# Performance work log

Hardware: AMD Instinct MI355X
Metric: run time of the kernel (lower is better)

Reference implementation:

```python
import jax, jax.numpy as jnp
import numpy as np

N_NODES = 20000
N_EDGES = 320000
IN_F = 256
OUT_F = 256
EDGE_F = 256


def _mlp2(x, W1, b1, W2, b2):
    # MLPLayers(2, [d_in, 2*d_in, d_out]) = Linear -> ReLU -> Linear
    return jax.nn.relu(x @ W1 + b1) @ W2 + b2


def setup_inputs() -> dict:
    key = jax.random.key(0)
    ks = jax.random.split(key, 12)

    def lin(k, fan_in, shape):
        bound = 1.0 / np.sqrt(fan_in)
        return jax.random.uniform(k, shape, jnp.float32, -bound, bound)

    node_feat = jax.random.normal(ks[0], (N_NODES, IN_F), jnp.float32)
    edge_feat = jax.random.normal(ks[1], (N_EDGES, EDGE_F), jnp.float32)
    src = jax.random.randint(ks[2], (N_EDGES,), 0, N_NODES, jnp.int32)
    dst = jax.random.randint(ks[3], (N_EDGES,), 0, N_NODES, jnp.int32)

    # edge_mlp: edge_feats -> 2*edge_feats -> in_feats
    We1 = lin(ks[4], EDGE_F, (EDGE_F, 2 * EDGE_F))
    be1 = lin(ks[5], EDGE_F, (2 * EDGE_F,))
    We2 = lin(ks[6], 2 * EDGE_F, (2 * EDGE_F, IN_F))
    be2 = lin(ks[7], 2 * EDGE_F, (IN_F,))
    # node mlp: in_feats -> 2*in_feats -> out_feats
    Wn1 = lin(ks[8], IN_F, (IN_F, 2 * IN_F))
    bn1 = lin(ks[9], IN_F, (2 * IN_F,))
    Wn2 = lin(ks[10], 2 * IN_F, (2 * IN_F, OUT_F))
    bn2 = lin(ks[11], 2 * IN_F, (OUT_F,))
    eps = jnp.zeros((1,), jnp.float32)

    return {"node_feat": node_feat, "edge_feat": edge_feat, "src": src, "dst": dst,
            "We1": We1, "be1": be1, "We2": We2, "be2": be2,
            "Wn1": Wn1, "bn1": bn1, "Wn2": Wn2, "bn2": bn2, "eps": eps}


def reference(node_feat, edge_feat, src, dst, We1, be1, We2, be2, Wn1, bn1, Wn2, bn2, eps):
    e = _mlp2(edge_feat, We1, be1, We2, be2)            # [E, IN_F]
    msg = jax.nn.relu(node_feat[src] + e)               # gather-add-relu
    out_h = jax.ops.segment_sum(msg, dst, num_segments=N_NODES)  # [N, IN_F]
    out = _mlp2((1.0 + eps[0]) * node_feat + out_h, Wn1, bn1, Wn2, bn2)
    return out
```

## Files before the change

kernel.cpp:

```cpp
#include <hip/hip_runtime.h>

#define NN  20000
#define NE  320000
#define FIN 256
#define FH  512

typedef __attribute__((ext_vector_type(8))) short bf16x8;
typedef __attribute__((ext_vector_type(4))) float f32x4;
typedef __attribute__((ext_vector_type(4))) unsigned short u16x4;

static __device__ __forceinline__ unsigned short f2b(float f) {
    union { float f; unsigned int i; } v; v.f = f;
    return (unsigned short)((v.i + 0x7fffu + ((v.i >> 16) & 1u)) >> 16);
}
static __device__ __forceinline__ f32x4 mfma16(bf16x8 a, bf16x8 b, f32x4 c) {
    return __builtin_amdgcn_mfma_f32_16x16x32_bf16(a, b, c, 0, 0, 0);
}
static __device__ __forceinline__ u16x4 pack4(float a, float b, float c, float d) {
    u16x4 p;
    p[0] = f2b(a); p[1] = f2b(b); p[2] = f2b(c); p[3] = f2b(d);
    return p;
}

__global__ void prep_weights(const float* __restrict__ We1, const float* __restrict__ We2,
                             const float* __restrict__ Wn1, const float* __restrict__ Wn2,
                             unsigned short* __restrict__ W1T, unsigned short* __restrict__ W2T,
                             unsigned short* __restrict__ Wn1T, unsigned short* __restrict__ Wn2T) {
    const int m = blockIdx.x >> 7;
    const int t = blockIdx.x & 127;
    const float* src; unsigned short* dst; int R, C;
    if      (m == 0) { src = We1; dst = W1T;  R = 256; C = 512; }
    else if (m == 1) { src = We2; dst = W2T;  R = 512; C = 256; }
    else if (m == 2) { src = Wn1; dst = Wn1T; R = 256; C = 512; }
    else             { src = Wn2; dst = Wn2T; R = 512; C = 256; }
    __shared__ unsigned short tl[32][33];
    const int tx  = threadIdx.x & 31;
    const int tyb = threadIdx.x >> 5;
    const int cb = C >> 5;
    const int bx = t % cb, by = t / cb;
    #pragma unroll
    for (int j = 0; j < 4; ++j)
        tl[tyb * 4 + j][tx] = f2b(src[(size_t)(by * 32 + tyb * 4 + j) * C + bx * 32 + tx]);
    __syncthreads();
    #pragma unroll
    for (int j = 0; j < 4; ++j)
        dst[(size_t)(bx * 32 + tyb * 4 + j) * R + by * 32 + tx] = tl[tx][tyb * 4 + j];
}

__global__ void hist_dst(const int* __restrict__ dstI, int* __restrict__ cnt) {
    int e = blockIdx.x * 256 + threadIdx.x;
    if (e < NE) atomicAdd(&cnt[dstI[e]], 1);
}

__global__ void scan_excl(const int* __restrict__ cnt, int* __restrict__ cursor) {
    __shared__ int c[NN];
    __shared__ int s[1024];
    const int t = threadIdx.x;
    for (int i = t; i < NN; i += 1024) c[i] = cnt[i];
    __syncthreads();
    const int lo = t * 20;
    const int hi = (lo + 20 < NN) ? lo + 20 : NN;
    int sum = 0;
    for (int i = lo; i < hi; ++i) sum += c[i];
    s[t] = sum;
    __syncthreads();
    for (int off = 1; off < 1024; off <<= 1) {
        int v = (t >= off) ? s[t - off] : 0;
        __syncthreads();
        s[t] += v;
        __syncthreads();
    }
    int base = (t > 0) ? s[t - 1] : 0;
    for (int i = lo; i < hi; ++i) { int cv = c[i]; c[i] = base; base += cv; }
    __syncthreads();
    for (int i = t; i < NN; i += 1024) cursor[i] = c[i];
}

__global__ void scatter_perm(const int* __restrict__ dstI,
                             int* __restrict__ cursor, int* __restrict__ perm) {
    int e = blockIdx.x * 256 + threadIdx.x;
    if (e < NE) {
        int pos = atomicAdd(&cursor[dstI[e]], 1);
        perm[pos] = e;
    }
}

__global__ void __launch_bounds__(512, 4)
gine_edge(const float* __restrict__ edge_feat,
          const float* __restrict__ node_feat,
          const int* __restrict__ srcI,
          const int* __restrict__ dstI,
          const int* __restrict__ perm,
          const unsigned short* __restrict__ W1T,
          const float* __restrict__ b1,
          const unsigned short* __restrict__ W2T,
          const float* __restrict__ b2,
          float* __restrict__ out_h)
{
    __shared__ union {
        unsigned short Xs[64 * 264];
        unsigned short Hs[64 * 512];
        float          Msg[64 * 260];
    } sh;
    __shared__ int snS[64], dnS[64], eS[64];

    const int tid  = threadIdx.x;
    const int wave = tid >> 6;
    const int lane = tid & 63;
    const int quad = lane >> 4;
    const int ln   = lane & 15;
    const int bs   = (blockIdx.x & 7) * 625 + (blockIdx.x >> 3);
    const int e0   = bs * 64;

    if (tid < 64) {
        const int e = perm[e0 + tid];
        eS[tid]  = e;
        snS[tid] = srcI[e];
        dnS[tid] = dstI[e];
    }
    __syncthreads();

    #pragma unroll
    for (int it = 0; it < 4; ++it) {
        const int chunk = tid + it * 512;
        const int row = chunk >> 5;
        const int c8  = (chunk & 31) << 3;
        const float* p = edge_feat + (size_t)eS[row] * FIN + c8;
        f32x4 o0 = *(const f32x4*)(p);
        f32x4 o1 = *(const f32x4*)(p + 4);
        bf16x8 pack;
        #pragma unroll
        for (int j = 0; j < 4; ++j) {
            pack[j]     = (short)f2b(o0[j]);
            pack[j + 4] = (short)f2b(o1[j]);
        }
        *(bf16x8*)(&sh.Xs[row * 264 + c8]) = pack;
    }
    __syncthreads();

    f32x4 zero4 = {0.f, 0.f, 0.f, 0.f};
    f32x4 acc1[4][4];
    #pragma unroll
    for (int nt = 0; nt < 4; ++nt)
        #pragma unroll
        for (int et = 0; et < 4; ++et) acc1[nt][et] = zero4;

    const unsigned short* wB = W1T + (wave * 64 + ln) * FIN + quad * 8;
    #pragma unroll
    for (int ks = 0; ks < 8; ++ks) {
        bf16x8 w[4], x[4];
        #pragma unroll
        for (int nt = 0; nt < 4; ++nt)
            w[nt] = *(const bf16x8*)(wB + nt * 16 * FIN + ks * 32);
        #pragma unroll
        for (int et = 0; et < 4; ++et)
            x[et] = *(const bf16x8*)(&sh.Xs[(et * 16 + ln) * 264 + quad * 8 + ks * 32]);
        #pragma unroll
        for (int nt = 0; nt < 4; ++nt)
            #pragma unroll
            for (int et = 0; et < 4; ++et)
                acc1[nt][et] = mfma16(w[nt], x[et], acc1[nt][et]);
    }
    __syncthreads();

    #pragma unroll
    for (int nt = 0; nt < 4; ++nt) {
        const int n0 = wave * 64 + nt * 16 + quad * 4;
        const f32x4 b4 = *(const f32x4*)(b1 + n0);
        #pragma unroll
        for (int et = 0; et < 4; ++et) {
            const int edge = et * 16 + ln;
            u16x4 p = pack4(fmaxf(acc1[nt][et][0] + b4[0], 0.f),
                            fmaxf(acc1[nt][et][1] + b4[1], 0.f),
                            fmaxf(acc1[nt][et][2] + b4[2], 0.f),
                            fmaxf(acc1[nt][et][3] + b4[3], 0.f));
            *(u16x4*)(&sh.Hs[(edge << 9) + (((n0 >> 3) ^ (edge & 7)) << 3) + (n0 & 7)]) = p;
        }
    }
    __syncthreads();

    f32x4 acc2[2][4];
    #pragma unroll
    for (int nt = 0; nt < 2; ++nt)
        #pragma unroll
        for (int et = 0; et < 4; ++et) acc2[nt][et] = zero4;

    const unsigned short* w2B = W2T + (wave * 32 + ln) * FH;
    #pragma unroll
    for (int ks = 0; ks < 16; ++ks) {
        const int kb = ks * 4 + quad;
        bf16x8 w[2], h[4];
        #pragma unroll
        for (int nt = 0; nt < 2; ++nt)
            w[nt] = *(const bf16x8*)(w2B + nt * 16 * FH + kb * 8);
        #pragma unroll
        for (int et = 0; et < 4; ++et) {
            const int edge = et * 16 + ln;
            h[et] = *(const bf16x8*)(&sh.Hs[(edge << 9) + ((kb ^ (edge & 7)) << 3)]);
        }
        #pragma unroll
        for (int nt = 0; nt < 2; ++nt)
            #pragma unroll
            for (int et = 0; et < 4; ++et)
                acc2[nt][et] = mfma16(w[nt], h[et], acc2[nt][et]);
    }
    __syncthreads();

    #pragma unroll
    for (int nt = 0; nt < 2; ++nt) {
        const int n0 = wave * 32 + nt * 16 + quad * 4;
        const f32x4 b4 = *(const f32x4*)(b2 + n0);
        #pragma unroll
        for (int et = 0; et < 4; ++et) {
            const int edge = et * 16 + ln;
            const int sn = snS[edge];
            const f32x4 nf = *(const f32x4*)(node_feat + (size_t)sn * FIN + n0);
            f32x4 m;
            #pragma unroll
            for (int r = 0; r < 4; ++r)
                m[r] = fmaxf(nf[r] + acc2[nt][et][r] + b4[r], 0.f);
            *(f32x4*)(&sh.Msg[edge * 260 + n0]) = m;
        }
    }
    __syncthreads();

    {
        const int col  = tid & 255;
        const int half = tid >> 8;
        const int rA   = half * 32;
        const int dF = dnS[rA], dL = dnS[rA + 31];
        float run = sh.Msg[rA * 260 + col];
        int cur = dF;
        #pragma unroll 4
        for (int row = rA + 1; row < rA + 32; ++row) {
            const int d = dnS[row];
            if (d != cur) {
                if (cur == dF || cur == dL)
                    atomicAdd(&out_h[(size_t)cur * FIN + col], run);
                else
                    out_h[(size_t)cur * FIN + col] = run;
                run = 0.f;
                cur = d;
            }
            run += sh.Msg[row * 260 + col];
        }
        atomicAdd(&out_h[(size_t)cur * FIN + col], run);
    }
}

__global__ void __launch_bounds__(512, 4)
gine_node(const float* __restrict__ node_feat,
          const float* __restrict__ out_h,
          const unsigned short* __restrict__ W1T,
          const float* __restrict__ b1,
          const unsigned short* __restrict__ W2T,
          const float* __restrict__ b2,
          const float* __restrict__ eps,
          float* __restrict__ out)
{
    __shared__ union {
        unsigned short Xs[64 * 264];
        unsigned short Hs[64 * 512];
    } sh;

    const int tid  = threadIdx.x;
    const int wave = tid >> 6;
    const int lane = tid & 63;
    const int quad = lane >> 4;
    const int ln   = lane & 15;
    const int n0b  = blockIdx.x * 64;
    const float epsv = 1.0f + eps[0];

    #pragma unroll
    for (int it = 0; it < 4; ++it) {
        const int chunk = tid + it * 512;
        const int row = chunk >> 5;
        const int c8  = (chunk & 31) << 3;
        const int g   = n0b + row;
        bf16x8 pack = {0, 0, 0, 0, 0, 0, 0, 0};
        if (g < NN) {
            const float* pn = node_feat + (size_t)g * FIN + c8;
            const float* ph = out_h + (size_t)g * FIN + c8;
            f32x4 n0v = *(const f32x4*)(pn);
            f32x4 n1v = *(const f32x4*)(pn + 4);
            f32x4 h0v = *(const f32x4*)(ph);
            f32x4 h1v = *(const f32x4*)(ph + 4);
            #pragma unroll
            for (int j = 0; j < 4; ++j) {
                pack[j]     = (short)f2b(epsv * n0v[j] + h0v[j]);
                pack[j + 4] = (short)f2b(epsv * n1v[j] + h1v[j]);
            }
        }
        *(bf16x8*)(&sh.Xs[row * 264 + c8]) = pack;
    }
    __syncthreads();

    f32x4 zero4 = {0.f, 0.f, 0.f, 0.f};
    f32x4 acc1[4][4];
    #pragma unroll
    for (int nt = 0; nt < 4; ++nt)
        #pragma unroll
        for (int et = 0; et < 4; ++et) acc1[nt][et] = zero4;

    const unsigned short* wB = W1T + (wave * 64 + ln) * FIN + quad * 8;
    #pragma unroll
    for (int ks = 0; ks < 8; ++ks) {
        bf16x8 w[4], x[4];
        #pragma unroll
        for (int nt = 0; nt < 4; ++nt)
            w[nt] = *(const bf16x8*)(wB + nt * 16 * FIN + ks * 32);
        #pragma unroll
        for (int et = 0; et < 4; ++et)
            x[et] = *(const bf16x8*)(&sh.Xs[(et * 16 + ln) * 264 + quad * 8 + ks * 32]);
        #pragma unroll
        for (int nt = 0; nt < 4; ++nt)
            #pragma unroll
            for (int et = 0; et < 4; ++et)
                acc1[nt][et] = mfma16(w[nt], x[et], acc1[nt][et]);
    }
    __syncthreads();

    #pragma unroll
    for (int nt = 0; nt < 4; ++nt) {
        const int n0 = wave * 64 + nt * 16 + quad * 4;
        const f32x4 b4 = *(const f32x4*)(b1 + n0);
        #pragma unroll
        for (int et = 0; et < 4; ++et) {
            const int edge = et * 16 + ln;
            u16x4 p = pack4(fmaxf(acc1[nt][et][0] + b4[0], 0.f),
                            fmaxf(acc1[nt][et][1] + b4[1], 0.f),
                            fmaxf(acc1[nt][et][2] + b4[2], 0.f),
                            fmaxf(acc1[nt][et][3] + b4[3], 0.f));
            *(u16x4*)(&sh.Hs[(edge << 9) + (((n0 >> 3) ^ (edge & 7)) << 3) + (n0 & 7)]) = p;
        }
    }
    __syncthreads();

    f32x4 acc2[2][4];
    #pragma unroll
    for (int nt = 0; nt < 2; ++nt)
        #pragma unroll
        for (int et = 0; et < 4; ++et) acc2[nt][et] = zero4;

    const unsigned short* w2B = W2T + (wave * 32 + ln) * FH;
    #pragma unroll
    for (int ks = 0; ks < 16; ++ks) {
        const int kb = ks * 4 + quad;
        bf16x8 w[2], h[4];
        #pragma unroll
        for (int nt = 0; nt < 2; ++nt)
            w[nt] = *(const bf16x8*)(w2B + nt * 16 * FH + kb * 8);
        #pragma unroll
        for (int et = 0; et < 4; ++et) {
            const int edge = et * 16 + ln;
            h[et] = *(const bf16x8*)(&sh.Hs[(edge << 9) + ((kb ^ (edge & 7)) << 3)]);
        }
        #pragma unroll
        for (int nt = 0; nt < 2; ++nt)
            #pragma unroll
            for (int et = 0; et < 4; ++et)
                acc2[nt][et] = mfma16(w[nt], h[et], acc2[nt][et]);
    }

    #pragma unroll
    for (int nt = 0; nt < 2; ++nt) {
        const int n0 = wave * 32 + nt * 16 + quad * 4;
        const f32x4 b4 = *(const f32x4*)(b2 + n0);
        #pragma unroll
        for (int et = 0; et < 4; ++et) {
            const int g = n0b + et * 16 + ln;
            if (g < NN) {
                f32x4 o;
                #pragma unroll
                for (int r = 0; r < 4; ++r)
                    o[r] = acc2[nt][et][r] + b4[r];
                *(f32x4*)(out + (size_t)g * FIN + n0) = o;
            }
        }
    }
}

extern "C" void kernel_launch(void* const* d_in, const int* in_sizes, int n_in,
                              void* d_out, int out_size, void* d_ws, size_t ws_size,
                              hipStream_t stream) {
    const float* node_feat = (const float*)d_in[0];
    const float* edge_feat = (const float*)d_in[1];
    const int* srcI = (const int*)d_in[2];
    const int* dstI = (const int*)d_in[3];
    const float* We1 = (const float*)d_in[4];
    const float* be1 = (const float*)d_in[5];
    const float* We2 = (const float*)d_in[6];
    const float* be2 = (const float*)d_in[7];
    const float* Wn1 = (const float*)d_in[8];
    const float* bn1 = (const float*)d_in[9];
    const float* Wn2 = (const float*)d_in[10];
    const float* bn2 = (const float*)d_in[11];
    const float* eps = (const float*)d_in[12];

    char* ws = (char*)d_ws;
    float* out_h = (float*)ws;
    unsigned short* W1T  = (unsigned short*)(ws + 20480000);
    unsigned short* W2T  = W1T + 131072;
    unsigned short* Wn1T = W2T + 131072;
    unsigned short* Wn2T = Wn1T + 131072;
    int* cnt    = (int*)(ws + 20480000 + 4 * 262144);
    int* cursor = cnt + NN;
    int* perm   = cursor + NN;

    hipMemsetAsync(out_h, 0, (size_t)NN * FIN * sizeof(float), stream);
    hipMemsetAsync(cnt, 0, NN * sizeof(int), stream);

    prep_weights<<<512, 256, 0, stream>>>(We1, We2, Wn1, Wn2, W1T, W2T, Wn1T, Wn2T);

    hist_dst<<<(NE + 255) / 256, 256, 0, stream>>>(dstI, cnt);
    scan_excl<<<1, 1024, 0, stream>>>(cnt, cursor);
    scatter_perm<<<(NE + 255) / 256, 256, 0, stream>>>(dstI, cursor, perm);

    gine_edge<<<NE / 64, 512, 0, stream>>>(edge_feat, node_feat, srcI, dstI,
                                           perm, W1T, be1, W2T, be2, out_h);
    gine_node<<<(NN + 63) / 64, 512, 0, stream>>>(node_feat, out_h, Wn1T, bn1,
                                                  Wn2T, bn2, eps, (float*)d_out);
}
```

Baseline: 870.5 us.

## Make edge kernel persistent with prefetched indices and direct fp32 edge-feature loads

The edge kernel becomes persistent: 512 blocks each loop over 9-10 tiles of 64 edges, and the next tile's perm/src/dst indices are prefetched into a double-buffered shared array. The shared Xs staging of edge features is removed. Each lane now loads its fp32 edge-feature slice straight from global memory and converts it in registers with packed bf16 conversion before the MFMA, which drops a shared round trip and a barrier. In exchange there are fewer resident blocks, so less latency hiding, and the gathered global loads become less coalesced (32-byte pieces per lane).

```diff
diff --git a/kernel.cpp b/kernel.cpp
--- a/kernel.cpp
+++ b/kernel.cpp
@@ -1,4 +1,5 @@
 #include <hip/hip_runtime.h>
+#include <hip/hip_bf16.h>
 
 #define NN  20000
 #define NE  320000
@@ -8,6 +9,7 @@
 typedef __attribute__((ext_vector_type(8))) short bf16x8;
 typedef __attribute__((ext_vector_type(4))) float f32x4;
 typedef __attribute__((ext_vector_type(4))) unsigned short u16x4;
+typedef __attribute__((ext_vector_type(4))) unsigned int u32x4;
 
 static __device__ __forceinline__ unsigned short f2b(float f) {
     union { float f; unsigned int i; } v; v.f = f;
@@ -20,6 +22,19 @@
     u16x4 p;
     p[0] = f2b(a); p[1] = f2b(b); p[2] = f2b(c); p[3] = f2b(d);
     return p;
+}
+static __device__ __forceinline__ unsigned int cvtpk(float lo, float hi) {
+    union { __hip_bfloat162 h; unsigned int u; } v;
+    v.h = __float22bfloat162_rn(float2{lo, hi});
+    return v.u;
+}
+static __device__ __forceinline__ bf16x8 cvt8(f32x4 a, f32x4 b) {
+    u32x4 t;
+    t[0] = cvtpk(a[0], a[1]);
+    t[1] = cvtpk(a[2], a[3]);
+    t[2] = cvtpk(b[0], b[1]);
+    t[3] = cvtpk(b[2], b[3]);
+    return __builtin_bit_cast(bf16x8, t);
 }
 
 __global__ void prep_weights(const float* __restrict__ We1, const float* __restrict__ We2,
@@ -98,153 +113,160 @@
           float* __restrict__ out_h)
 {
     __shared__ union {
-        unsigned short Xs[64 * 264];
         unsigned short Hs[64 * 512];
         float          Msg[64 * 260];
     } sh;
-    __shared__ int snS[64], dnS[64], eS[64];
+    __shared__ int snS[2][64], dnS[2][64], eS[2][64];
 
     const int tid  = threadIdx.x;
     const int wave = tid >> 6;
     const int lane = tid & 63;
     const int quad = lane >> 4;
     const int ln   = lane & 15;
-    const int bs   = (blockIdx.x & 7) * 625 + (blockIdx.x >> 3);
-    const int e0   = bs * 64;
+
+    const int x = blockIdx.x & 7;
+    const int j = blockIdx.x >> 3;
+    const int off   = (j < 49) ? j * 10 : 490 + (j - 49) * 9;
+    const int ntile = (j < 49) ? 10 : 9;
+    const int t0    = x * 625 + off;
 
     if (tid < 64) {
-        const int e = perm[e0 + tid];
-        eS[tid]  = e;
-        snS[tid] = srcI[e];
-        dnS[tid] = dstI[e];
-    }
-    __syncthreads();
-
-    #pragma unroll
-    for (int it = 0; it < 4; ++it) {
-        const int chunk = tid + it * 512;
-        const int row = chunk >> 5;
-        const int c8  = (chunk & 31) << 3;
-        const float* p = edge_feat + (size_t)eS[row] * FIN + c8;
-        f32x4 o0 = *(const f32x4*)(p);
-        f32x4 o1 = *(const f32x4*)(p + 4);
-        bf16x8 pack;
-        #pragma unroll
-        for (int j = 0; j < 4; ++j) {
-            pack[j]     = (short)f2b(o0[j]);
-            pack[j + 4] = (short)f2b(o1[j]);
-        }
-        *(bf16x8*)(&sh.Xs[row * 264 + c8]) = pack;
-    }
-    __syncthreads();
-
-    f32x4 zero4 = {0.f, 0.f, 0.f, 0.f};
-    f32x4 acc1[4][4];
-    #pragma unroll
-    for (int nt = 0; nt < 4; ++nt)
-        #pragma unroll
-        for (int et = 0; et < 4; ++et) acc1[nt][et] = zero4;
-
-    const unsigned short* wB = W1T + (wave * 64 + ln) * FIN + quad * 8;
-    #pragma unroll
-    for (int ks = 0; ks < 8; ++ks) {
-        bf16x8 w[4], x[4];
+        const int e = perm[t0 * 64 + tid];
+        eS[0][tid] = e; snS[0][tid] = srcI[e]; dnS[0][tid] = dstI[e];
+    }
+    __syncthreads();
+
+    const unsigned short* wB  = W1T + (wave * 64 + ln) * FIN + quad * 8;
+    const unsigned short* w2B = W2T + (wave * 32 + ln) * FH;
+    const f32x4 zero4 = {0.f, 0.f, 0.f, 0.f};
+
+    for (int i = 0; i < ntile; ++i) {
+        const int p  = i & 1;
+        const int q  = p ^ 1;
+
+        int eN = 0, sN = 0, dN = 0;
+        const bool pf = (tid < 64) && (i + 1 < ntile);
+        if (pf) {
+            eN = perm[(t0 + i + 1) * 64 + tid];
+            sN = srcI[eN];
+            dN = dstI[eN];
+        }
+
+        const float* xb[4];
+        #pragma unroll
+        for (int et = 0; et < 4; ++et)
+            xb[et] = edge_feat + (size_t)eS[p][et * 16 + ln] * FIN + quad * 8;
+
+        f32x4 acc1[4][4];
         #pragma unroll
         for (int nt = 0; nt < 4; ++nt)
-            w[nt] = *(const bf16x8*)(wB + nt * 16 * FIN + ks * 32);
-        #pragma unroll
-        for (int et = 0; et < 4; ++et)
-            x[et] = *(const bf16x8*)(&sh.Xs[(et * 16 + ln) * 264 + quad * 8 + ks * 32]);
-        #pragma unroll
-        for (int nt = 0; nt < 4; ++nt)
-            #pragma unroll
-            for (int et = 0; et < 4; ++et)
-                acc1[nt][et] = mfma16(w[nt], x[et], acc1[nt][et]);
-    }
-    __syncthreads();
-
-    #pragma unroll
-    for (int nt = 0; nt < 4; ++nt) {
-        const int n0 = wave * 64 + nt * 16 + quad * 4;
-        const f32x4 b4 = *(const f32x4*)(b1 + n0);
-        #pragma unroll
-        for (int et = 0; et < 4; ++et) {
-            const int edge = et * 16 + ln;
-            u16x4 p = pack4(fmaxf(acc1[nt][et][0] + b4[0], 0.f),
-                            fmaxf(acc1[nt][et][1] + b4[1], 0.f),
-                            fmaxf(acc1[nt][et][2] + b4[2], 0.f),
-                            fmaxf(acc1[nt][et][3] + b4[3], 0.f));
-            *(u16x4*)(&sh.Hs[(edge << 9) + (((n0 >> 3) ^ (edge & 7)) << 3) + (n0 & 7)]) = p;
-        }
-    }
-    __syncthreads();
-
-    f32x4 acc2[2][4];
-    #pragma unroll
-    for (int nt = 0; nt < 2; ++nt)
-        #pragma unroll
-        for (int et = 0; et < 4; ++et) acc2[nt][et] = zero4;
-
-    const unsigned short* w2B = W2T + (wave * 32 + ln) * FH;
-    #pragma unroll
-    for (int ks = 0; ks < 16; ++ks) {
-        const int kb = ks * 4 + quad;
-        bf16x8 w[2], h[4];
+            #pragma unroll
+            for (int et = 0; et < 4; ++et) acc1[nt][et] = zero4;
+
+        #pragma unroll
+        for (int ks = 0; ks < 8; ++ks) {
+            bf16x8 w[4], xf[4];
+            #pragma unroll
+            for (int nt = 0; nt < 4; ++nt)
+                w[nt] = *(const bf16x8*)(wB + nt * 16 * FIN + ks * 32);
+            #pragma unroll
+            for (int et = 0; et < 4; ++et) {
+                const f32x4 a = *(const f32x4*)(xb[et] + ks * 32);
+                const f32x4 b = *(const f32x4*)(xb[et] + ks * 32 + 4);
+                xf[et] = cvt8(a, b);
+            }
+            #pragma unroll
+            for (int nt = 0; nt < 4; ++nt)
+                #pragma unroll
+                for (int et = 0; et < 4; ++et)
+                    acc1[nt][et] = mfma16(w[nt], xf[et], acc1[nt][et]);
+        }
+
+        if (pf) { eS[q][tid] = eN; snS[q][tid] = sN; dnS[q][tid] = dN; }
+
+        #pragma unroll
+        for (int nt = 0; nt < 4; ++nt) {
+            const int n0 = wave * 64 + nt * 16 + quad * 4;
+            const f32x4 b4 = *(const f32x4*)(b1 + n0);
+            #pragma unroll
+            for (int et = 0; et < 4; ++et) {
+                const int edge = et * 16 + ln;
+                u16x4 pk = pack4(fmaxf(acc1[nt][et][0] + b4[0], 0.f),
+                                 fmaxf(acc1[nt][et][1] + b4[1], 0.f),
+                                 fmaxf(acc1[nt][et][2] + b4[2], 0.f),
+                                 fmaxf(acc1[nt][et][3] + b4[3], 0.f));
+                *(u16x4*)(&sh.Hs[(edge << 9) + (((n0 >> 3) ^ (edge & 7)) << 3) + (n0 & 7)]) = pk;
+            }
+        }
+        __syncthreads();
+
+        f32x4 acc2[2][4];
         #pragma unroll
         for (int nt = 0; nt < 2; ++nt)
-            w[nt] = *(const bf16x8*)(w2B + nt * 16 * FH + kb * 8);
-        #pragma unroll
-        for (int et = 0; et < 4; ++et) {
-            const int edge = et * 16 + ln;
-            h[et] = *(const bf16x8*)(&sh.Hs[(edge << 9) + ((kb ^ (edge & 7)) << 3)]);
-        }
-        #pragma unroll
-        for (int nt = 0; nt < 2; ++nt)
-            #pragma unroll
-            for (int et = 0; et < 4; ++et)
-                acc2[nt][et] = mfma16(w[nt], h[et], acc2[nt][et]);
-    }
-    __syncthreads();
-
-    #pragma unroll
-    for (int nt = 0; nt < 2; ++nt) {
-        const int n0 = wave * 32 + nt * 16 + quad * 4;
-        const f32x4 b4 = *(const f32x4*)(b2 + n0);
-        #pragma unroll
-        for (int et = 0; et < 4; ++et) {
-            const int edge = et * 16 + ln;
-            const int sn = snS[edge];
-            const f32x4 nf = *(const f32x4*)(node_feat + (size_t)sn * FIN + n0);
-            f32x4 m;
-            #pragma unroll
-            for (int r = 0; r < 4; ++r)
-                m[r] = fmaxf(nf[r] + acc2[nt][et][r] + b4[r], 0.f);
-            *(f32x4*)(&sh.Msg[edge * 260 + n0]) = m;
-        }
-    }
-    __syncthreads();
-
-    {
-        const int col  = tid & 255;
-        const int half = tid >> 8;
-        const int rA   = half * 32;
-        const int dF = dnS[rA], dL = dnS[rA + 31];
-        float run = sh.Msg[rA * 260 + col];
-        int cur = dF;
-        #pragma unroll 4
-        for (int row = rA + 1; row < rA + 32; ++row) {
-            const int d = dnS[row];
-            if (d != cur) {
-                if (cur == dF || cur == dL)
-                    atomicAdd(&out_h[(size_t)cur * FIN + col], run);
-                else
-                    out_h[(size_t)cur * FIN + col] = run;
-                run = 0.f;
-                cur = d;
-            }
-            run += sh.Msg[row * 260 + col];
-        }
-        atomicAdd(&out_h[(size_t)cur * FIN + col], run);
+            #pragma unroll
+            for (int et = 0; et < 4; ++et) acc2[nt][et] = zero4;
+
+        #pragma unroll
+        for (int ks = 0; ks < 16; ++ks) {
+            const int kb = ks * 4 + quad;
+            bf16x8 w[2], h[4];
+            #pragma unroll
+            for (int nt = 0; nt < 2; ++nt)
+                w[nt] = *(const bf16x8*)(w2B + nt * 16 * FH + kb * 8);
+            #pragma unroll
+            for (int et = 0; et < 4; ++et) {
+                const int edge = et * 16 + ln;
+                h[et] = *(const bf16x8*)(&sh.Hs[(edge << 9) + ((kb ^ (edge & 7)) << 3)]);
+            }
+            #pragma unroll
+            for (int nt = 0; nt < 2; ++nt)
+                #pragma unroll
+                for (int et = 0; et < 4; ++et)
+                    acc2[nt][et] = mfma16(w[nt], h[et], acc2[nt][et]);
+        }
+        __syncthreads();
+
+        #pragma unroll
+        for (int nt = 0; nt < 2; ++nt) {
+            const int n0 = wave * 32 + nt * 16 + quad * 4;
+            const f32x4 b4 = *(const f32x4*)(b2 + n0);
+            #pragma unroll
+            for (int et = 0; et < 4; ++et) {
+                const int edge = et * 16 + ln;
+                const int sn = snS[p][edge];
+                const f32x4 nf = *(const f32x4*)(node_feat + (size_t)sn * FIN + n0);
+                f32x4 m;
+                #pragma unroll
+                for (int r = 0; r < 4; ++r)
+                    m[r] = fmaxf(nf[r] + acc2[nt][et][r] + b4[r], 0.f);
+                *(f32x4*)(&sh.Msg[edge * 260 + n0]) = m;
+            }
+        }
+        __syncthreads();
+
+        {
+            const int col  = tid & 255;
+            const int half = tid >> 8;
+            const int rA   = half * 32;
+            const int dF = dnS[p][rA], dL = dnS[p][rA + 31];
+            float run = sh.Msg[rA * 260 + col];
+            int cur = dF;
+            #pragma unroll 4
+            for (int row = rA + 1; row < rA + 32; ++row) {
+                const int d = dnS[p][row];
+                if (d != cur) {
+                    if (cur == dF || cur == dL)
+                        atomicAdd(&out_h[(size_t)cur * FIN + col], run);
+                    else
+                        out_h[(size_t)cur * FIN + col] = run;
+                    run = 0.f;
+                    cur = d;
+                }
+                run += sh.Msg[row * 260 + col];
+            }
+            atomicAdd(&out_h[(size_t)cur * FIN + col], run);
+        }
+        __syncthreads();
     }
 }
 
@@ -305,18 +327,18 @@
     const unsigned short* wB = W1T + (wave * 64 + ln) * FIN + quad * 8;
     #pragma unroll
     for (int ks = 0; ks < 8; ++ks) {
-        bf16x8 w[4], x[4];
+        bf16x8 w[4], xv[4];
         #pragma unroll
         for (int nt = 0; nt < 4; ++nt)
             w[nt] = *(const bf16x8*)(wB + nt * 16 * FIN + ks * 32);
         #pragma unroll
         for (int et = 0; et < 4; ++et)
-            x[et] = *(const bf16x8*)(&sh.Xs[(et * 16 + ln) * 264 + quad * 8 + ks * 32]);
+            xv[et] = *(const bf16x8*)(&sh.Xs[(et * 16 + ln) * 264 + quad * 8 + ks * 32]);
         #pragma unroll
         for (int nt = 0; nt < 4; ++nt)
             #pragma unroll
             for (int et = 0; et < 4; ++et)
-                acc1[nt][et] = mfma16(w[nt], x[et], acc1[nt][et]);
+                acc1[nt][et] = mfma16(w[nt], xv[et], acc1[nt][et]);
     }
     __syncthreads();
 
@@ -327,11 +349,11 @@
         #pragma unroll
         for (int et = 0; et < 4; ++et) {
             const int edge = et * 16 + ln;
-            u16x4 p = pack4(fmaxf(acc1[nt][et][0] + b4[0], 0.f),
-                            fmaxf(acc1[nt][et][1] + b4[1], 0.f),
-                            fmaxf(acc1[nt][et][2] + b4[2], 0.f),
-                            fmaxf(acc1[nt][et][3] + b4[3], 0.f));
-            *(u16x4*)(&sh.Hs[(edge << 9) + (((n0 >> 3) ^ (edge & 7)) << 3) + (n0 & 7)]) = p;
+            u16x4 pk = pack4(fmaxf(acc1[nt][et][0] + b4[0], 0.f),
+                             fmaxf(acc1[nt][et][1] + b4[1], 0.f),
+                             fmaxf(acc1[nt][et][2] + b4[2], 0.f),
+                             fmaxf(acc1[nt][et][3] + b4[3], 0.f));
+            *(u16x4*)(&sh.Hs[(edge << 9) + (((n0 >> 3) ^ (edge & 7)) << 3) + (n0 & 7)]) = pk;
         }
     }
     __syncthreads();
@@ -416,8 +438,8 @@
     scan_excl<<<1, 1024, 0, stream>>>(cnt, cursor);
     scatter_perm<<<(NE + 255) / 256, 256, 0, stream>>>(dstI, cursor, perm);
 
-    gine_edge<<<NE / 64, 512, 0, stream>>>(edge_feat, node_feat, srcI, dstI,
-                                           perm, W1T, be1, W2T, be2, out_h);
+    gine_edge<<<512, 512, 0, stream>>>(edge_feat, node_feat, srcI, dstI,
+                                       perm, W1T, be1, W2T, be2, out_h);
     gine_node<<<(NN + 63) / 64, 512, 0, stream>>>(node_feat, out_h, Wn1T, bn1,
                                                   Wn2T, bn2, eps, (float*)d_out);
 }
```

Measured after the change: 1.469 ms. 68.7% more time.

## Split hidden dimension into halves to shrink LDS and raise occupancy

Applied to the files above, without the earlier changes.

Both the edge and node MLP kernels now process the 512-wide hidden layer in two 256-wide halves, accumulating the second GEMM across halves. This halves the hidden-activation shared buffer and the first-layer accumulator registers. The message buffer is also processed in two 32-edge passes, so launch bounds can request 8 blocks per CU instead of 4. The input tile is cached in registers (xr[8][4]) and reused across halves, and the float-to-bf16 conversion now uses the packed hardware conversion intrinsic. The risks are extra barriers, re-reading W1 per half, and register pressure from holding the input tile.

```diff
diff --git a/kernel.cpp b/kernel.cpp
--- a/kernel.cpp
+++ b/kernel.cpp
@@ -1,4 +1,5 @@
 #include <hip/hip_runtime.h>
+#include <hip/hip_bf16.h>
 
 #define NN  20000
 #define NE  320000
@@ -8,6 +9,7 @@
 typedef __attribute__((ext_vector_type(8))) short bf16x8;
 typedef __attribute__((ext_vector_type(4))) float f32x4;
 typedef __attribute__((ext_vector_type(4))) unsigned short u16x4;
+typedef __attribute__((ext_vector_type(4))) unsigned int u32x4;
 
 static __device__ __forceinline__ unsigned short f2b(float f) {
     union { float f; unsigned int i; } v; v.f = f;
@@ -16,10 +18,23 @@
 static __device__ __forceinline__ f32x4 mfma16(bf16x8 a, bf16x8 b, f32x4 c) {
     return __builtin_amdgcn_mfma_f32_16x16x32_bf16(a, b, c, 0, 0, 0);
 }
+static __device__ __forceinline__ unsigned int cvtpk(float lo, float hi) {
+    union { __hip_bfloat162 h; unsigned int u; } v;
+    v.h = __float22bfloat162_rn(float2{lo, hi});
+    return v.u;
+}
 static __device__ __forceinline__ u16x4 pack4(float a, float b, float c, float d) {
-    u16x4 p;
-    p[0] = f2b(a); p[1] = f2b(b); p[2] = f2b(c); p[3] = f2b(d);
-    return p;
+    union { u16x4 s; unsigned int u[2]; } v;
+    v.u[0] = cvtpk(a, b); v.u[1] = cvtpk(c, d);
+    return v.s;
+}
+static __device__ __forceinline__ bf16x8 cvt8(f32x4 a, f32x4 b) {
+    u32x4 t;
+    t[0] = cvtpk(a[0], a[1]);
+    t[1] = cvtpk(a[2], a[3]);
+    t[2] = cvtpk(b[0], b[1]);
+    t[3] = cvtpk(b[2], b[3]);
+    return __builtin_bit_cast(bf16x8, t);
 }
 
 __global__ void prep_weights(const float* __restrict__ We1, const float* __restrict__ We2,
@@ -85,7 +100,7 @@
     }
 }
 
-__global__ void __launch_bounds__(512, 4)
+__global__ void __launch_bounds__(512, 8)
 gine_edge(const float* __restrict__ edge_feat,
           const float* __restrict__ node_feat,
           const int* __restrict__ srcI,
@@ -99,8 +114,8 @@
 {
     __shared__ union {
         unsigned short Xs[64 * 264];
-        unsigned short Hs[64 * 512];
-        float          Msg[64 * 260];
+        unsigned short Hs[64 * 256];
+        float          Msg[32 * 264];
     } sh;
     __shared__ int snS[64], dnS[64], eS[64];
 
@@ -128,127 +143,132 @@
         const float* p = edge_feat + (size_t)eS[row] * FIN + c8;
         f32x4 o0 = *(const f32x4*)(p);
         f32x4 o1 = *(const f32x4*)(p + 4);
-        bf16x8 pack;
-        #pragma unroll
-        for (int j = 0; j < 4; ++j) {
-            pack[j]     = (short)f2b(o0[j]);
-            pack[j + 4] = (short)f2b(o1[j]);
-        }
-        *(bf16x8*)(&sh.Xs[row * 264 + c8]) = pack;
-    }
-    __syncthreads();
-
-    f32x4 zero4 = {0.f, 0.f, 0.f, 0.f};
-    f32x4 acc1[4][4];
-    #pragma unroll
-    for (int nt = 0; nt < 4; ++nt)
-        #pragma unroll
-        for (int et = 0; et < 4; ++et) acc1[nt][et] = zero4;
-
-    const unsigned short* wB = W1T + (wave * 64 + ln) * FIN + quad * 8;
-    #pragma unroll
-    for (int ks = 0; ks < 8; ++ks) {
-        bf16x8 w[4], x[4];
-        #pragma unroll
-        for (int nt = 0; nt < 4; ++nt)
-            w[nt] = *(const bf16x8*)(wB + nt * 16 * FIN + ks * 32);
+        *(bf16x8*)(&sh.Xs[row * 264 + c8]) = cvt8(o0, o1);
+    }
+    __syncthreads();
+
+    bf16x8 xr[8][4];
+    #pragma unroll
+    for (int ks = 0; ks < 8; ++ks)
         #pragma unroll
         for (int et = 0; et < 4; ++et)
-            x[et] = *(const bf16x8*)(&sh.Xs[(et * 16 + ln) * 264 + quad * 8 + ks * 32]);
-        #pragma unroll
-        for (int nt = 0; nt < 4; ++nt)
-            #pragma unroll
-            for (int et = 0; et < 4; ++et)
-                acc1[nt][et] = mfma16(w[nt], x[et], acc1[nt][et]);
-    }
-    __syncthreads();
-
-    #pragma unroll
-    for (int nt = 0; nt < 4; ++nt) {
-        const int n0 = wave * 64 + nt * 16 + quad * 4;
-        const f32x4 b4 = *(const f32x4*)(b1 + n0);
-        #pragma unroll
-        for (int et = 0; et < 4; ++et) {
-            const int edge = et * 16 + ln;
-            u16x4 p = pack4(fmaxf(acc1[nt][et][0] + b4[0], 0.f),
-                            fmaxf(acc1[nt][et][1] + b4[1], 0.f),
-                            fmaxf(acc1[nt][et][2] + b4[2], 0.f),
-                            fmaxf(acc1[nt][et][3] + b4[3], 0.f));
-            *(u16x4*)(&sh.Hs[(edge << 9) + (((n0 >> 3) ^ (edge & 7)) << 3) + (n0 & 7)]) = p;
-        }
-    }
-    __syncthreads();
-
+            xr[ks][et] = *(const bf16x8*)(&sh.Xs[(et * 16 + ln) * 264 + quad * 8 + ks * 32]);
+    __syncthreads();
+
+    const f32x4 zero4 = {0.f, 0.f, 0.f, 0.f};
     f32x4 acc2[2][4];
     #pragma unroll
     for (int nt = 0; nt < 2; ++nt)
         #pragma unroll
         for (int et = 0; et < 4; ++et) acc2[nt][et] = zero4;
 
-    const unsigned short* w2B = W2T + (wave * 32 + ln) * FH;
-    #pragma unroll
-    for (int ks = 0; ks < 16; ++ks) {
-        const int kb = ks * 4 + quad;
-        bf16x8 w[2], h[4];
+    #pragma unroll
+    for (int h = 0; h < 2; ++h) {
+        f32x4 acc1[2][4];
         #pragma unroll
         for (int nt = 0; nt < 2; ++nt)
-            w[nt] = *(const bf16x8*)(w2B + nt * 16 * FH + kb * 8);
-        #pragma unroll
-        for (int et = 0; et < 4; ++et) {
-            const int edge = et * 16 + ln;
-            h[et] = *(const bf16x8*)(&sh.Hs[(edge << 9) + ((kb ^ (edge & 7)) << 3)]);
-        }
-        #pragma unroll
-        for (int nt = 0; nt < 2; ++nt)
-            #pragma unroll
-            for (int et = 0; et < 4; ++et)
-                acc2[nt][et] = mfma16(w[nt], h[et], acc2[nt][et]);
-    }
-    __syncthreads();
-
-    #pragma unroll
-    for (int nt = 0; nt < 2; ++nt) {
-        const int n0 = wave * 32 + nt * 16 + quad * 4;
-        const f32x4 b4 = *(const f32x4*)(b2 + n0);
-        #pragma unroll
-        for (int et = 0; et < 4; ++et) {
-            const int edge = et * 16 + ln;
-            const int sn = snS[edge];
-            const f32x4 nf = *(const f32x4*)(node_feat + (size_t)sn * FIN + n0);
-            f32x4 m;
-            #pragma unroll
-            for (int r = 0; r < 4; ++r)
-                m[r] = fmaxf(nf[r] + acc2[nt][et][r] + b4[r], 0.f);
-            *(f32x4*)(&sh.Msg[edge * 260 + n0]) = m;
-        }
-    }
-    __syncthreads();
-
-    {
-        const int col  = tid & 255;
-        const int half = tid >> 8;
-        const int rA   = half * 32;
-        const int dF = dnS[rA], dL = dnS[rA + 31];
-        float run = sh.Msg[rA * 260 + col];
-        int cur = dF;
-        #pragma unroll 4
-        for (int row = rA + 1; row < rA + 32; ++row) {
-            const int d = dnS[row];
-            if (d != cur) {
-                if (cur == dF || cur == dL)
-                    atomicAdd(&out_h[(size_t)cur * FIN + col], run);
-                else
-                    out_h[(size_t)cur * FIN + col] = run;
-                run = 0.f;
-                cur = d;
-            }
-            run += sh.Msg[row * 260 + col];
-        }
-        atomicAdd(&out_h[(size_t)cur * FIN + col], run);
-    }
-}
-
-__global__ void __launch_bounds__(512, 4)
+            #pragma unroll
+            for (int et = 0; et < 4; ++et) acc1[nt][et] = zero4;
+
+        const unsigned short* wB = W1T + (size_t)(h * 256 + wave * 32 + ln) * FIN + quad * 8;
+        #pragma unroll
+        for (int ks = 0; ks < 8; ++ks) {
+            bf16x8 w1[2];
+            #pragma unroll
+            for (int nt = 0; nt < 2; ++nt)
+                w1[nt] = *(const bf16x8*)(wB + nt * 16 * FIN + ks * 32);
+            #pragma unroll
+            for (int nt = 0; nt < 2; ++nt)
+                #pragma unroll
+                for (int et = 0; et < 4; ++et)
+                    acc1[nt][et] = mfma16(w1[nt], xr[ks][et], acc1[nt][et]);
+        }
+
+        #pragma unroll
+        for (int nt = 0; nt < 2; ++nt) {
+            const int nl = wave * 32 + nt * 16 + quad * 4;
+            const f32x4 b4 = *(const f32x4*)(b1 + h * 256 + nl);
+            #pragma unroll
+            for (int et = 0; et < 4; ++et) {
+                const int edge = et * 16 + ln;
+                u16x4 pk = pack4(fmaxf(acc1[nt][et][0] + b4[0], 0.f),
+                                 fmaxf(acc1[nt][et][1] + b4[1], 0.f),
+                                 fmaxf(acc1[nt][et][2] + b4[2], 0.f),
+                                 fmaxf(acc1[nt][et][3] + b4[3], 0.f));
+                *(u16x4*)(&sh.Hs[(edge << 8) + (((nl >> 3) ^ (edge & 7)) << 3) + (nl & 7)]) = pk;
+            }
+        }
+        __syncthreads();
+
+        const unsigned short* w2B = W2T + (size_t)(wave * 32 + ln) * FH + h * 256;
+        #pragma unroll
+        for (int ks = 0; ks < 8; ++ks) {
+            const int kb = ks * 4 + quad;
+            bf16x8 w2[2], hf[4];
+            #pragma unroll
+            for (int nt = 0; nt < 2; ++nt)
+                w2[nt] = *(const bf16x8*)(w2B + nt * 16 * FH + kb * 8);
+            #pragma unroll
+            for (int et = 0; et < 4; ++et) {
+                const int edge = et * 16 + ln;
+                hf[et] = *(const bf16x8*)(&sh.Hs[(edge << 8) + ((kb ^ (edge & 7)) << 3)]);
+            }
+            #pragma unroll
+            for (int nt = 0; nt < 2; ++nt)
+                #pragma unroll
+                for (int et = 0; et < 4; ++et)
+                    acc2[nt][et] = mfma16(w2[nt], hf[et], acc2[nt][et]);
+        }
+        __syncthreads();
+    }
+
+    #pragma unroll
+    for (int eh = 0; eh < 2; ++eh) {
+        #pragma unroll
+        for (int nt = 0; nt < 2; ++nt) {
+            const int n0 = wave * 32 + nt * 16 + quad * 4;
+            const f32x4 b4 = *(const f32x4*)(b2 + n0);
+            #pragma unroll
+            for (int el = 0; el < 2; ++el) {
+                const int et = eh * 2 + el;
+                const int edge = et * 16 + ln;
+                const int sn = snS[edge];
+                const f32x4 nf = *(const f32x4*)(node_feat + (size_t)sn * FIN + n0);
+                f32x4 m;
+                #pragma unroll
+                for (int r = 0; r < 4; ++r)
+                    m[r] = fmaxf(nf[r] + acc2[nt][et][r] + b4[r], 0.f);
+                *(f32x4*)(&sh.Msg[(el * 16 + ln) * 264 + n0]) = m;
+            }
+        }
+        __syncthreads();
+
+        if (tid < 256) {
+            const int col = tid;
+            const int rA = eh * 32;
+            const int dF = dnS[rA], dL = dnS[rA + 31];
+            float run = sh.Msg[col];
+            int cur = dF;
+            #pragma unroll 4
+            for (int row = 1; row < 32; ++row) {
+                const int d = dnS[rA + row];
+                if (d != cur) {
+                    if (cur == dF || cur == dL)
+                        atomicAdd(&out_h[(size_t)cur * FIN + col], run);
+                    else
+                        out_h[(size_t)cur * FIN + col] = run;
+                    run = 0.f;
+                    cur = d;
+                }
+                run += sh.Msg[row * 264 + col];
+            }
+            atomicAdd(&out_h[(size_t)cur * FIN + col], run);
+        }
+        __syncthreads();
+    }
+}
+
+__global__ void __launch_bounds__(512, 8)
 gine_node(const float* __restrict__ node_feat,
           const float* __restrict__ out_h,
           const unsigned short* __restrict__ W1T,
@@ -260,7 +280,7 @@
 {
     __shared__ union {
         unsigned short Xs[64 * 264];
-        unsigned short Hs[64 * 512];
+        unsigned short Hs[64 * 256];
     } sh;
 
     const int tid  = threadIdx.x;
@@ -285,81 +305,91 @@
             f32x4 n1v = *(const f32x4*)(pn + 4);
             f32x4 h0v = *(const f32x4*)(ph);
             f32x4 h1v = *(const f32x4*)(ph + 4);
+            f32x4 a, b;
             #pragma unroll
             for (int j = 0; j < 4; ++j) {
-                pack[j]     = (short)f2b(epsv * n0v[j] + h0v[j]);
-                pack[j + 4] = (short)f2b(epsv * n1v[j] + h1v[j]);
-            }
+                a[j] = epsv * n0v[j] + h0v[j];
+                b[j] = epsv * n1v[j] + h1v[j];
+            }
+            pack = cvt8(a, b);
         }
         *(bf16x8*)(&sh.Xs[row * 264 + c8]) = pack;
     }
     __syncthreads();
 
-    f32x4 zero4 = {0.f, 0.f, 0.f, 0.f};
-    f32x4 acc1[4][4];
-    #pragma unroll
-    for (int nt = 0; nt < 4; ++nt)
-        #pragma unroll
-        for (int et = 0; et < 4; ++et) acc1[nt][et] = zero4;
-
-    const unsigned short* wB = W1T + (wave * 64 + ln) * FIN + quad * 8;
-    #pragma unroll
-    for (int ks = 0; ks < 8; ++ks) {
-        bf16x8 w[4], x[4];
-        #pragma unroll
-        for (int nt = 0; nt < 4; ++nt)
-            w[nt] = *(const bf16x8*)(wB + nt * 16 * FIN + ks * 32);
+    bf16x8 xr[8][4];
+    #pragma unroll
+    for (int ks = 0; ks < 8; ++ks)
         #pragma unroll
         for (int et = 0; et < 4; ++et)
-            x[et] = *(const bf16x8*)(&sh.Xs[(et * 16 + ln) * 264 + quad * 8 + ks * 32]);
-        #pragma unroll
-        for (int nt = 0; nt < 4; ++nt)
-            #pragma unroll
-            for (int et = 0; et < 4; ++et)
-                acc1[nt][et] = mfma16(w[nt], x[et], acc1[nt][et]);
-    }
-    __syncthreads();
-
-    #pragma unroll
-    for (int nt = 0; nt < 4; ++nt) {
-        const int n0 = wave * 64 + nt * 16 + quad * 4;
-        const f32x4 b4 = *(const f32x4*)(b1 + n0);
-        #pragma unroll
-        for (int et = 0; et < 4; ++et) {
-            const int edge = et * 16 + ln;
-            u16x4 p = pack4(fmaxf(acc1[nt][et][0] + b4[0], 0.f),
-                            fmaxf(acc1[nt][et][1] + b4[1], 0.f),
-                            fmaxf(acc1[nt][et][2] + b4[2], 0.f),
-                            fmaxf(acc1[nt][et][3] + b4[3], 0.f));
-            *(u16x4*)(&sh.Hs[(edge << 9) + (((n0 >> 3) ^ (edge & 7)) << 3) + (n0 & 7)]) = p;
-        }
-    }
-    __syncthreads();
-
+            xr[ks][et] = *(const bf16x8*)(&sh.Xs[(et * 16 + ln) * 264 + quad * 8 + ks * 32]);
+    __syncthreads();
+
+    const f32x4 zero4 = {0.f, 0.f, 0.f, 0.f};
     f32x4 acc2[2][4];
     #pragma unroll
     for (int nt = 0; nt < 2; ++nt)
         #pragma unroll
         for (int et = 0; et < 4; ++et) acc2[nt][et] = zero4;
 
-    const unsigned short* w2B = W2T + (wave * 32 + ln) * FH;
-    #pragma unroll
-    for (int ks = 0; ks < 16; ++ks) {
-        const int kb = ks * 4 + quad;
-        bf16x8 w[2], h[4];
+    #pragma unroll
+    for (int h = 0; h < 2; ++h) {
+        f32x4 acc1[2][4];
         #pragma unroll
         for (int nt = 0; nt < 2; ++nt)
-            w[nt] = *(const bf16x8*)(w2B + nt * 16 * FH + kb * 8);
-        #pragma unroll
-        for (int et = 0; et < 4; ++et) {
-            const int edge = et * 16 + ln;
-            h[et] = *(const bf16x8*)(&sh.Hs[(edge << 9) + ((kb ^ (edge & 7)) << 3)]);
-        }
-        #pragma unroll
-        for (int nt = 0; nt < 2; ++nt)
-            #pragma unroll
-            for (int et = 0; et < 4; ++et)
-                acc2[nt][et] = mfma16(w[nt], h[et], acc2[nt][et]);
+            #pragma unroll
+            for (int et = 0; et < 4; ++et) acc1[nt][et] = zero4;
+
+        const unsigned short* wB = W1T + (size_t)(h * 256 + wave * 32 + ln) * FIN + quad * 8;
+        #pragma unroll
+        for (int ks = 0; ks < 8; ++ks) {
+            bf16x8 w1[2];
+            #pragma unroll
+            for (int nt = 0; nt < 2; ++nt)
+                w1[nt] = *(const bf16x8*)(wB + nt * 16 * FIN + ks * 32);
+            #pragma unroll
+            for (int nt = 0; nt < 2; ++nt)
+                #pragma unroll
+                for (int et = 0; et < 4; ++et)
+                    acc1[nt][et] = mfma16(w1[nt], xr[ks][et], acc1[nt][et]);
+        }
+
+        #pragma unroll
+        for (int nt = 0; nt < 2; ++nt) {
+            const int nl = wave * 32 + nt * 16 + quad * 4;
+            const f32x4 b4 = *(const f32x4*)(b1 + h * 256 + nl);
+            #pragma unroll
+            for (int et = 0; et < 4; ++et) {
+                const int edge = et * 16 + ln;
+                u16x4 pk = pack4(fmaxf(acc1[nt][et][0] + b4[0], 0.f),
+                                 fmaxf(acc1[nt][et][1] + b4[1], 0.f),
+                                 fmaxf(acc1[nt][et][2] + b4[2], 0.f),
+                                 fmaxf(acc1[nt][et][3] + b4[3], 0.f));
+                *(u16x4*)(&sh.Hs[(edge << 8) + (((nl >> 3) ^ (edge & 7)) << 3) + (nl & 7)]) = pk;
+            }
+        }
+        __syncthreads();
+
+        const unsigned short* w2B = W2T + (size_t)(wave * 32 + ln) * FH + h * 256;
+        #pragma unroll
+        for (int ks = 0; ks < 8; ++ks) {
+            const int kb = ks * 4 + quad;
+            bf16x8 w2[2], hf[4];
+            #pragma unroll
+            for (int nt = 0; nt < 2; ++nt)
+                w2[nt] = *(const bf16x8*)(w2B + nt * 16 * FH + kb * 8);
+            #pragma unroll
+            for (int et = 0; et < 4; ++et) {
+                const int edge = et * 16 + ln;
+                hf[et] = *(const bf16x8*)(&sh.Hs[(edge << 8) + ((kb ^ (edge & 7)) << 3)]);
+            }
+            #pragma unroll
+            for (int nt = 0; nt < 2; ++nt)
+                #pragma unroll
+                for (int et = 0; et < 4; ++et)
+                    acc2[nt][et] = mfma16(w2[nt], hf[et], acc2[nt][et]);
+        }
+        __syncthreads();
     }
 
     #pragma unroll
```

New measurement: 2.261 ms. 2.6x slower.
